# Kernel tuning notes

Measured on AMD Instinct MI355X. Metric: run time of the kernel, lower is better.

The kernel has to match this reference:

```python
import jax, jax.numpy as jnp
import numpy as np

B, C, H, W = 8, 1024, 56, 56
NBINS = 256          # torch.histc(bins=256, min=0, max=1)
T_THRESH = 0.9       # EKLM entropy-ratio threshold
NUM_CLASSES = 30


def setup_inputs() -> dict:
    key = jax.random.key(0)
    k1, k2 = jax.random.split(key)
    x = jax.random.uniform(k1, (B, C, H, W), dtype=jnp.float32)
    w_fc = jax.random.normal(k2, (C, NUM_CLASSES), dtype=jnp.float32) * 0.02
    return {"x": x, "w_fc": w_fc}


def _integral_hist(x):
    """One fused pass replacing the per-region torch.histc calls.
    Returns per-(h,w)-cell histograms [H,W,256] and their 2D inclusive
    prefix sum padded to [H+1,W+1,256] so any rectangle histogram is 4 lookups.
    Matches torch.histc semantics: values outside [0,1] ignored, v==1 -> last bin."""
    valid = (x >= 0.0) & (x <= 1.0)
    q = jnp.clip(jnp.floor(x * NBINS), 0, NBINS - 1).astype(jnp.int32)
    q = jnp.where(valid, q, NBINS)  # out-of-range -> extra bin, dropped below
    hh = jnp.broadcast_to(jnp.arange(H)[None, None, :, None], x.shape)
    ww = jnp.broadcast_to(jnp.arange(W)[None, None, None, :], x.shape)
    cell = jnp.zeros((H, W, NBINS + 1), jnp.float32).at[hh, ww, q].add(1.0)[..., :NBINS]
    integ = jnp.cumsum(jnp.cumsum(cell, axis=0), axis=1)
    integ = jnp.pad(integ, ((1, 0), (1, 0), (0, 0)))  # [H+1, W+1, 256]
    return cell, integ


def _entropy_of_hist(h):
    p = h / jnp.sum(h)
    return -jnp.sum(p * jnp.log2(p + 1e-9))


def _region_entropy(integ, xs, xd, ys, yd):
    # histogram of x[:, :, xs:xd, ys:yd] via integral-histogram lookups
    h = integ[xd, yd] - integ[xs, yd] - integ[xd, ys] + integ[xs, ys]
    return _entropy_of_hist(h)


def eklm(x):
    """Entropy-based Key Localization Method (xs fixed to 0, as in source)."""
    cell, integ = _integral_hist(x)
    # compute_entropy_for_each_y: entropy of each [:, :, 0:1, y:y+1] column cell
    col_hists = cell[0]  # [W, 256]
    p = col_hists / jnp.sum(col_hists, axis=1, keepdims=True)
    ent_y = -jnp.sum(p * jnp.log2(p + 1e-9), axis=1)
    ys0 = jnp.argmax(ent_y).astype(jnp.int32)
    total_ent = _region_entropy(integ, 0, H, 0, W)

    def ent(xd, ys, yd):
        return _region_entropy(integ, 0, xd, ys, yd)

    def cond(state):
        xd, ys, yd, Ts, done = state
        return (Ts < T_THRESH) & (~done)

    def body(state):
        xd, ys, yd, Ts, done = state
        e_cur = ent(xd, ys, yd)
        # greedy priority identical to source: grow xd, else shrink ys, else grow yd
        c1 = (xd + 1 < H) & (ent(xd + 1, ys, yd) > e_cur)
        c2 = (~c1) & (ys - 1 >= 0) & (ent(xd, jnp.maximum(ys - 1, 0), yd) > e_cur)
        c3 = (~c1) & (~c2) & (yd + 1 < W) & (ent(xd, ys, jnp.minimum(yd + 1, W)) > e_cur)
        xd_n = jnp.where(c1, xd + 1, xd)
        ys_n = jnp.where(c2, ys - 1, ys)
        yd_n = jnp.where(c3, yd + 1, yd)
        done_n = ~(c1 | c2 | c3)
        Ts_n = ent(xd_n, ys_n, yd_n) / total_ent
        return (xd_n, ys_n, yd_n, Ts_n, done_n)

    xd0 = jnp.int32(1)
    yd0 = ys0 + jnp.int32(1)
    Ts0 = ent(xd0, ys0, yd0) / total_ent
    xd, ys, yd, _, _ = jax.lax.while_loop(
        cond, body, (xd0, ys0, yd0, Ts0, jnp.bool_(False)))
    return jnp.int32(0), xd, ys, yd


def reference(x, w_fc):
    xs, xd, ys, yd = eklm(x)
    # crop the located key region (mask form for static shapes), mean-pool, classify
    row = jnp.arange(H)
    col = jnp.arange(W)
    mask = ((row[:, None] >= xs) & (row[:, None] < xd)
            & (col[None, :] >= ys) & (col[None, :] < yd)).astype(x.dtype)
    area = jnp.maximum(jnp.sum(mask), 1.0)
    pooled = jnp.einsum('bchw,hw->bc', x, mask) / area  # [B, C]
    return pooled @ w_fc  # [B, NUM_CLASSES]
```

## Files before the change

### kernel.cpp

```cpp
#include <hip/hip_runtime.h>
#include <math.h>

#define BB 8
#define CC 1024
#define HH 56
#define WW 56
#define NB 256
#define NCLS 30
#define BC (BB * CC)
#define PLANE (HH * WW)
#define NWORD (NB / 2)
#define CELLW (HH * WW * NWORD)
#define SLICES 16
#define WSPLIT 2
#define WHALF (WW / WSPLIT)
#define PL_PER_SLICE (BC / SLICES)
#define HTHREADS 256
#define VEC4_PER_BLOCK (PL_PER_SLICE * WHALF / 4)
#define LH_WORDS (WHALF * NWORD)

template <bool ATOMIC_FLUSH>
__global__ __launch_bounds__(HTHREADS) void hist_kernel(const float* __restrict__ x,
                                                        unsigned* __restrict__ dst) {
    __shared__ unsigned lh[LH_WORDS];
    const int tid = threadIdx.x;
    const int bid = blockIdx.x;
    const int whalf = bid & (WSPLIT - 1);
    const int hs = bid / WSPLIT;
    const int h = hs % HH;
    const int slice = hs / HH;

    for (int i = tid; i < LH_WORDS; i += HTHREADS) lh[i] = 0u;
    __syncthreads();

    const float* __restrict__ xb =
        x + (size_t)(slice * PL_PER_SLICE) * PLANE + h * WW + whalf * WHALF;

#pragma unroll
    for (int it = 0; it < VEC4_PER_BLOCK / HTHREADS; ++it) {
        const int j = it * HTHREADS + tid;
        const int bcl = j / 7;
        const int wq = j - bcl * 7;
        const float4 v = *(const float4*)(xb + (size_t)bcl * PLANE + wq * 4);
        const float vv[4] = {v.x, v.y, v.z, v.w};
#pragma unroll
        for (int e = 0; e < 4; ++e) {
            const float f = vv[e];
            if (f >= 0.f && f <= 1.f) {
                int bin = (int)(f * 256.f);
                if (bin > 255) bin = 255;
                const int wl = wq * 4 + e;
                atomicAdd(&lh[wl * NWORD + (bin >> 1)], 1u << ((bin & 1) << 4));
            }
        }
    }
    __syncthreads();

    if (ATOMIC_FLUSH) {
        unsigned* g = dst + ((size_t)h * WW + whalf * WHALF) * NWORD;
        for (int i = tid; i < LH_WORDS; i += HTHREADS) {
            const unsigned v = lh[i];
            if (v) atomicAdd(&g[i], v);
        }
    } else {
        unsigned* g = dst + ((size_t)hs * WW + whalf * WHALF) * NWORD;
        for (int i = tid; i < LH_WORDS; i += HTHREADS) g[i] = lh[i];
    }
}

__global__ void reduce_kernel(const unsigned* __restrict__ ps,
                              unsigned* __restrict__ hist) {
    const int idx = blockIdx.x * 256 + threadIdx.x;
    unsigned s = 0;
#pragma unroll
    for (int sl = 0; sl < SLICES; ++sl) s += ps[(size_t)sl * CELLW + idx];
    ((uint2*)hist)[idx] = make_uint2(s & 0xffffu, s >> 16);
}

__global__ void unpack_kernel(const unsigned* __restrict__ hp,
                              unsigned* __restrict__ hist) {
    const int idx = blockIdx.x * 256 + threadIdx.x;
    const unsigned s = hp[idx];
    ((uint2*)hist)[idx] = make_uint2(s & 0xffffu, s >> 16);
}

__global__ void cumw_kernel(unsigned* __restrict__ hist) {
    const int h = blockIdx.x, b = threadIdx.x;
    unsigned* base = hist + (size_t)h * WW * NB + b;
    unsigned v[WW];
#pragma unroll
    for (int w = 0; w < WW; ++w) v[w] = base[(size_t)w * NB];
    unsigned c = 0;
#pragma unroll
    for (int w = 0; w < WW; ++w) { c += v[w]; base[(size_t)w * NB] = c; }
}

__global__ void cumh_kernel(unsigned* __restrict__ hist) {
    const int w = blockIdx.x, b = threadIdx.x;
    unsigned* base = hist + (size_t)w * NB + b;
    unsigned v[HH];
#pragma unroll
    for (int h = 0; h < HH; ++h) v[h] = base[(size_t)h * WW * NB];
    unsigned c = 0;
#pragma unroll
    for (int h = 0; h < HH; ++h) { c += v[h]; base[(size_t)h * WW * NB] = c; }
}

__device__ __forceinline__ float wave_sum(float v) {
#pragma unroll
    for (int off = 32; off > 0; off >>= 1) v += __shfl_xor(v, off);
    return v;
}

__device__ __forceinline__ float ilook(const unsigned* __restrict__ integ,
                                       int a, int b, int bin) {
    return (a == 0 || b == 0)
               ? 0.f
               : (float)integ[((size_t)((a - 1) * WW + (b - 1))) * NB + bin];
}

__device__ float region_ent(const unsigned* __restrict__ integ, int lane,
                            int xd, int ys, int yd) {
    float hb[4];
    float hs = 0.f;
#pragma unroll
    for (int k = 0; k < 4; k++) {
        const int bin = lane + 64 * k;
        const float hv = ilook(integ, xd, yd, bin) - ilook(integ, xd, ys, bin);
        hb[k] = hv;
        hs += hv;
    }
    hs = wave_sum(hs);
    float e = 0.f;
#pragma unroll
    for (int k = 0; k < 4; k++) {
        const float p = hb[k] / hs;
        e += p * log2f(p + 1e-9f);
    }
    return -wave_sum(e);
}

__global__ __launch_bounds__(1024) void decide_kernel(const unsigned* __restrict__ integ,
                                                      int* __restrict__ region) {
    __shared__ float ent_s[WW];
    const int tid = threadIdx.x;
    const int lane = tid & 63;
    const int wv = tid >> 6;

    for (int w = wv; w < WW; w += 16) {
        float hb[4], hs = 0.f;
#pragma unroll
        for (int k = 0; k < 4; k++) {
            const int bin = lane + 64 * k;
            const float a = (float)integ[(size_t)w * NB + bin];
            const float b = w ? (float)integ[(size_t)(w - 1) * NB + bin] : 0.f;
            hb[k] = a - b;
            hs += hb[k];
        }
        hs = wave_sum(hs);
        float e = 0.f;
#pragma unroll
        for (int k = 0; k < 4; k++) {
            const float p = hb[k] / hs;
            e += p * log2f(p + 1e-9f);
        }
        e = -wave_sum(e);
        if (lane == 0) ent_s[w] = e;
    }
    __syncthreads();
    if (wv != 0) return;

    float best = -3.0e38f;
    int bestw = 0;
    for (int w = 0; w < WW; ++w) {
        const float e = ent_s[w];
        if (e > best) { best = e; bestw = w; }
    }

    const float total_ent = region_ent(integ, lane, HH, 0, WW);

    int xd = 1, ys = bestw, yd = bestw + 1;
    float Ts = region_ent(integ, lane, xd, ys, yd) / total_ent;
    bool done = false;
    int iter = 0;
    while (Ts < 0.9f && !done && iter < 1000) {
        iter++;
        const float e_cur = region_ent(integ, lane, xd, ys, yd);
        const int ysm = (ys - 1 < 0) ? 0 : ys - 1;
        const int ydp = (yd + 1 > WW) ? WW : yd + 1;
        const bool c1 = (xd + 1 < HH) && (region_ent(integ, lane, xd + 1, ys, yd) > e_cur);
        const bool c2 = !c1 && (ys - 1 >= 0) && (region_ent(integ, lane, xd, ysm, yd) > e_cur);
        const bool c3 = !c1 && !c2 && (yd + 1 < WW) && (region_ent(integ, lane, xd, ys, ydp) > e_cur);
        if (c1) xd = xd + 1;
        else if (c2) ys = ys - 1;
        else if (c3) yd = yd + 1;
        done = !(c1 || c2 || c3);
        Ts = region_ent(integ, lane, xd, ys, yd) / total_ent;
    }

    if (lane == 0) {
        region[0] = xd;
        region[1] = ys;
        region[2] = yd;
    }
}

__global__ void pool_kernel(const float* __restrict__ x,
                            const int* __restrict__ region,
                            float* __restrict__ pooled) {
    const int bc = blockIdx.x;
    const int xd = region[0], ys = region[1], yd = region[2];
    const int Wd = yd - ys;
    const int n = xd * Wd;
    const float area = fmaxf((float)n, 1.f);
    const float* plane = x + (size_t)bc * PLANE;
    float s = 0.f;
    for (int j = threadIdx.x; j < n; j += 64) {
        const int r = j / Wd;
        const int cc = ys + (j - r * Wd);
        s += plane[r * WW + cc];
    }
#pragma unroll
    for (int off = 32; off > 0; off >>= 1) s += __shfl_xor(s, off);
    if (threadIdx.x == 0) pooled[bc] = s / area;
}

__global__ __launch_bounds__(256) void fc_kernel(const float* __restrict__ pooled,
                                                 const float* __restrict__ wfc,
                                                 float* __restrict__ out) {
    __shared__ float red[240];
    const int b = blockIdx.x;
    const int t = threadIdx.x;
    if (t < 240) {
        const int chunk = t / NCLS;
        const int n = t - chunk * NCLS;
        const float* pv = pooled + b * CC + chunk * 128;
        const float* wv = wfc + (size_t)(chunk * 128) * NCLS + n;
        float a0 = 0.f, a1 = 0.f, a2 = 0.f, a3 = 0.f;
        for (int c = 0; c < 128; c += 4) {
            a0 += pv[c + 0] * wv[(c + 0) * NCLS];
            a1 += pv[c + 1] * wv[(c + 1) * NCLS];
            a2 += pv[c + 2] * wv[(c + 2) * NCLS];
            a3 += pv[c + 3] * wv[(c + 3) * NCLS];
        }
        red[t] = (a0 + a1) + (a2 + a3);
    }
    __syncthreads();
    if (t < NCLS) {
        float s = 0.f;
#pragma unroll
        for (int ch = 0; ch < 8; ++ch) s += red[ch * NCLS + t];
        out[b * NCLS + t] = s;
    }
}

extern "C" void kernel_launch(void* const* d_in, const int* in_sizes, int n_in,
                              void* d_out, int out_size, void* d_ws, size_t ws_size,
                              hipStream_t stream) {
    const float* x = (const float*)d_in[0];
    const float* wfc = (const float*)d_in[1];
    float* out = (float*)d_out;

    unsigned char* ws = (unsigned char*)d_ws;
    const size_t ps_bytes = (size_t)SLICES * CELLW * 4;
    const size_t hist_bytes = (size_t)CELLW * 8;
    const size_t needA = ps_bytes + hist_bytes + 4096 + (size_t)BC * 4;

    if (ws_size >= needA) {
        unsigned* ps = (unsigned*)ws;
        unsigned* hist = (unsigned*)(ws + ps_bytes);
        int* region = (int*)(ws + ps_bytes + hist_bytes);
        float* pooled = (float*)(ws + ps_bytes + hist_bytes + 4096);

        hist_kernel<false><<<HH * WSPLIT * SLICES, HTHREADS, 0, stream>>>(x, ps);
        reduce_kernel<<<CELLW / 256, 256, 0, stream>>>(ps, hist);
        cumw_kernel<<<HH, NB, 0, stream>>>(hist);
        cumh_kernel<<<WW, NB, 0, stream>>>(hist);
        decide_kernel<<<1, 1024, 0, stream>>>(hist, region);
        pool_kernel<<<BC, 64, 0, stream>>>(x, region, pooled);
        fc_kernel<<<BB, 256, 0, stream>>>(pooled, wfc, out);
    } else {
        unsigned* hp = (unsigned*)ws;
        unsigned* hist = (unsigned*)(ws + (size_t)CELLW * 4);
        int* region = (int*)(ws + (size_t)CELLW * 4 + hist_bytes);
        float* pooled = (float*)(ws + (size_t)CELLW * 4 + hist_bytes + 4096);

        hipMemsetAsync(hp, 0, (size_t)CELLW * 4, stream);
        hist_kernel<true><<<HH * WSPLIT * SLICES, HTHREADS, 0, stream>>>(x, hp);
        unpack_kernel<<<CELLW / 256, 256, 0, stream>>>(hp, hist);
        cumw_kernel<<<HH, NB, 0, stream>>>(hist);
        cumh_kernel<<<WW, NB, 0, stream>>>(hist);
        decide_kernel<<<1, 1024, 0, stream>>>(hist, region);
        pool_kernel<<<BC, 64, 0, stream>>>(x, region, pooled);
        fc_kernel<<<BB, 256, 0, stream>>>(pooled, wfc, out);
    }
}
```

Before: 187.8 us.

## Add early-exit fast path using row-0 column and global histograms

Replaces the full per-cell integral histogram build with one pass that accumulates only the row-0 per-column histograms plus a global 256-bin histogram. When the initial single-cell region already meets the entropy threshold, the search is skipped and the full integral-histogram work is avoided. Otherwise a cooperative fallback kernel rebuilds the full integral histogram with grid syncs and runs the search. The pooling kernel is also restructured for tiny regions. This trades a guaranteed full build for a data-dependent shortcut. If the ghist pass runs and the fallback still fires, it adds extra work, and the small-workspace path has no fallback at all.

```diff
diff --git a/kernel.cpp b/kernel.cpp
--- a/kernel.cpp
+++ b/kernel.cpp
@@ -1,5 +1,8 @@
 #include <hip/hip_runtime.h>
+#include <hip/hip_cooperative_groups.h>
 #include <math.h>
+
+namespace cg = cooperative_groups;
 
 #define BB 8
 #define CC 1024
@@ -10,38 +13,37 @@
 #define BC (BB * CC)
 #define PLANE (HH * WW)
 #define NWORD (NB / 2)
-#define CELLW (HH * WW * NWORD)
+#define CELLW (PLANE * NWORD)
 #define SLICES 16
-#define WSPLIT 2
-#define WHALF (WW / WSPLIT)
 #define PL_PER_SLICE (BC / SLICES)
-#define HTHREADS 256
-#define VEC4_PER_BLOCK (PL_PER_SLICE * WHALF / 4)
-#define LH_WORDS (WHALF * NWORD)
-
-template <bool ATOMIC_FLUSH>
-__global__ __launch_bounds__(HTHREADS) void hist_kernel(const float* __restrict__ x,
-                                                        unsigned* __restrict__ dst) {
-    __shared__ unsigned lh[LH_WORDS];
+
+#define FULL_NEED 28934400ull
+#define FAST_NEED 63488ull
+
+__global__ void zero_kernel(unsigned* __restrict__ p) {
+    const int i = blockIdx.x * 256 + threadIdx.x;
+    p[i] = 0u;
+}
+
+__global__ __launch_bounds__(256) void ghist_kernel(const float* __restrict__ x,
+                                                    unsigned* __restrict__ colhist,
+                                                    unsigned* __restrict__ ghist) {
+    __shared__ unsigned ch[HH * NWORD];
+    __shared__ unsigned gh[NB];
     const int tid = threadIdx.x;
-    const int bid = blockIdx.x;
-    const int whalf = bid & (WSPLIT - 1);
-    const int hs = bid / WSPLIT;
-    const int h = hs % HH;
-    const int slice = hs / HH;
-
-    for (int i = tid; i < LH_WORDS; i += HTHREADS) lh[i] = 0u;
+    for (int i = tid; i < HH * NWORD; i += 256) ch[i] = 0u;
+    gh[tid] = 0u;
     __syncthreads();
 
-    const float* __restrict__ xb =
-        x + (size_t)(slice * PL_PER_SLICE) * PLANE + h * WW + whalf * WHALF;
-
-#pragma unroll
-    for (int it = 0; it < VEC4_PER_BLOCK / HTHREADS; ++it) {
-        const int j = it * HTHREADS + tid;
-        const int bcl = j / 7;
-        const int wq = j - bcl * 7;
-        const float4 v = *(const float4*)(xb + (size_t)bcl * PLANE + wq * 4);
+    const float4* __restrict__ xb =
+        (const float4*)(x + (size_t)blockIdx.x * (16 * PLANE));
+    for (int it = 0; it < 49; ++it) {
+        const int j = it * 256 + tid;
+        const float4 v = xb[j];
+        const int e0 = j * 4;
+        const int pl = e0 / PLANE;
+        const int li = e0 - pl * PLANE;
+        const bool r0 = (li < WW);
         const float vv[4] = {v.x, v.y, v.z, v.w};
 #pragma unroll
         for (int e = 0; e < 4; ++e) {
@@ -49,61 +51,19 @@
             if (f >= 0.f && f <= 1.f) {
                 int bin = (int)(f * 256.f);
                 if (bin > 255) bin = 255;
-                const int wl = wq * 4 + e;
-                atomicAdd(&lh[wl * NWORD + (bin >> 1)], 1u << ((bin & 1) << 4));
+                atomicAdd(&gh[bin], 1u);
+                if (r0)
+                    atomicAdd(&ch[(li + e) * NWORD + (bin >> 1)],
+                              1u << ((bin & 1) << 4));
             }
         }
     }
     __syncthreads();
-
-    if (ATOMIC_FLUSH) {
-        unsigned* g = dst + ((size_t)h * WW + whalf * WHALF) * NWORD;
-        for (int i = tid; i < LH_WORDS; i += HTHREADS) {
-            const unsigned v = lh[i];
-            if (v) atomicAdd(&g[i], v);
-        }
-    } else {
-        unsigned* g = dst + ((size_t)hs * WW + whalf * WHALF) * NWORD;
-        for (int i = tid; i < LH_WORDS; i += HTHREADS) g[i] = lh[i];
-    }
-}
-
-__global__ void reduce_kernel(const unsigned* __restrict__ ps,
-                              unsigned* __restrict__ hist) {
-    const int idx = blockIdx.x * 256 + threadIdx.x;
-    unsigned s = 0;
-#pragma unroll
-    for (int sl = 0; sl < SLICES; ++sl) s += ps[(size_t)sl * CELLW + idx];
-    ((uint2*)hist)[idx] = make_uint2(s & 0xffffu, s >> 16);
-}
-
-__global__ void unpack_kernel(const unsigned* __restrict__ hp,
-                              unsigned* __restrict__ hist) {
-    const int idx = blockIdx.x * 256 + threadIdx.x;
-    const unsigned s = hp[idx];
-    ((uint2*)hist)[idx] = make_uint2(s & 0xffffu, s >> 16);
-}
-
-__global__ void cumw_kernel(unsigned* __restrict__ hist) {
-    const int h = blockIdx.x, b = threadIdx.x;
-    unsigned* base = hist + (size_t)h * WW * NB + b;
-    unsigned v[WW];
-#pragma unroll
-    for (int w = 0; w < WW; ++w) v[w] = base[(size_t)w * NB];
-    unsigned c = 0;
-#pragma unroll
-    for (int w = 0; w < WW; ++w) { c += v[w]; base[(size_t)w * NB] = c; }
-}
-
-__global__ void cumh_kernel(unsigned* __restrict__ hist) {
-    const int w = blockIdx.x, b = threadIdx.x;
-    unsigned* base = hist + (size_t)w * NB + b;
-    unsigned v[HH];
-#pragma unroll
-    for (int h = 0; h < HH; ++h) v[h] = base[(size_t)h * WW * NB];
-    unsigned c = 0;
-#pragma unroll
-    for (int h = 0; h < HH; ++h) { c += v[h]; base[(size_t)h * WW * NB] = c; }
+    for (int i = tid; i < HH * NWORD; i += 256) {
+        const unsigned v = ch[i];
+        if (v) atomicAdd(&colhist[i], v);
+    }
+    { const unsigned v = gh[tid]; if (v) atomicAdd(&ghist[tid], v); }
 }
 
 __device__ __forceinline__ float wave_sum(float v) {
@@ -140,8 +100,9 @@
     return -wave_sum(e);
 }
 
-__global__ __launch_bounds__(1024) void decide_kernel(const unsigned* __restrict__ integ,
-                                                      int* __restrict__ region) {
+__global__ __launch_bounds__(1024) void decide_fast_kernel(
+    const unsigned* __restrict__ colhist, const unsigned* __restrict__ ghist,
+    int* __restrict__ region, unsigned* __restrict__ flag) {
     __shared__ float ent_s[WW];
     const int tid = threadIdx.x;
     const int lane = tid & 63;
@@ -152,9 +113,8 @@
 #pragma unroll
         for (int k = 0; k < 4; k++) {
             const int bin = lane + 64 * k;
-            const float a = (float)integ[(size_t)w * NB + bin];
-            const float b = w ? (float)integ[(size_t)(w - 1) * NB + bin] : 0.f;
-            hb[k] = a - b;
+            const unsigned wd = colhist[w * NWORD + (bin >> 1)];
+            hb[k] = (float)((wd >> ((bin & 1) << 4)) & 0xffffu);
             hs += hb[k];
         }
         hs = wave_sum(hs);
@@ -177,52 +137,169 @@
         if (e > best) { best = e; bestw = w; }
     }
 
-    const float total_ent = region_ent(integ, lane, HH, 0, WW);
-
-    int xd = 1, ys = bestw, yd = bestw + 1;
-    float Ts = region_ent(integ, lane, xd, ys, yd) / total_ent;
-    bool done = false;
-    int iter = 0;
-    while (Ts < 0.9f && !done && iter < 1000) {
-        iter++;
-        const float e_cur = region_ent(integ, lane, xd, ys, yd);
-        const int ysm = (ys - 1 < 0) ? 0 : ys - 1;
-        const int ydp = (yd + 1 > WW) ? WW : yd + 1;
-        const bool c1 = (xd + 1 < HH) && (region_ent(integ, lane, xd + 1, ys, yd) > e_cur);
-        const bool c2 = !c1 && (ys - 1 >= 0) && (region_ent(integ, lane, xd, ysm, yd) > e_cur);
-        const bool c3 = !c1 && !c2 && (yd + 1 < WW) && (region_ent(integ, lane, xd, ys, ydp) > e_cur);
-        if (c1) xd = xd + 1;
-        else if (c2) ys = ys - 1;
-        else if (c3) yd = yd + 1;
-        done = !(c1 || c2 || c3);
-        Ts = region_ent(integ, lane, xd, ys, yd) / total_ent;
-    }
-
+    float hb[4], hs = 0.f;
+#pragma unroll
+    for (int k = 0; k < 4; k++) {
+        const int bin = lane + 64 * k;
+        hb[k] = (float)ghist[bin];
+        hs += hb[k];
+    }
+    hs = wave_sum(hs);
+    float e = 0.f;
+#pragma unroll
+    for (int k = 0; k < 4; k++) {
+        const float p = hb[k] / hs;
+        e += p * log2f(p + 1e-9f);
+    }
+    const float total_ent = -wave_sum(e);
+
+    const float Ts0 = best / total_ent;
     if (lane == 0) {
-        region[0] = xd;
-        region[1] = ys;
-        region[2] = yd;
-    }
-}
-
-__global__ void pool_kernel(const float* __restrict__ x,
-                            const int* __restrict__ region,
-                            float* __restrict__ pooled) {
-    const int bc = blockIdx.x;
+        region[0] = 1;
+        region[1] = bestw;
+        region[2] = bestw + 1;
+        *flag = (Ts0 >= 0.9f) ? 1u : 2u;
+    }
+}
+
+__global__ __launch_bounds__(256) void fallback_kernel(
+    const float* __restrict__ x, unsigned* __restrict__ ps,
+    unsigned* __restrict__ hist, int* __restrict__ region,
+    const unsigned* __restrict__ flag) {
+    if (*flag == 1u) return;
+    cg::grid_group grid = cg::this_grid();
+    __shared__ unsigned lh[HH * NWORD];
+    const int tid = threadIdx.x;
+    const int gtid = blockIdx.x * 256 + tid;
+
+    for (int t = blockIdx.x; t < HH * SLICES; t += 256) {
+        const int h = t % HH;
+        const int slice = t / HH;
+        for (int i = tid; i < HH * NWORD; i += 256) lh[i] = 0u;
+        __syncthreads();
+        const float* __restrict__ xb =
+            x + (size_t)(slice * PL_PER_SLICE) * PLANE + h * WW;
+        for (int it = 0; it < 28; ++it) {
+            const int j = it * 256 + tid;
+            const int bcl = j / 14;
+            const int wq = j - bcl * 14;
+            const float4 v = *(const float4*)(xb + (size_t)bcl * PLANE + wq * 4);
+            const float vv[4] = {v.x, v.y, v.z, v.w};
+#pragma unroll
+            for (int e = 0; e < 4; ++e) {
+                const float f = vv[e];
+                if (f >= 0.f && f <= 1.f) {
+                    int bin = (int)(f * 256.f);
+                    if (bin > 255) bin = 255;
+                    atomicAdd(&lh[(wq * 4 + e) * NWORD + (bin >> 1)],
+                              1u << ((bin & 1) << 4));
+                }
+            }
+        }
+        __syncthreads();
+        unsigned* g = ps + (size_t)slice * CELLW + (size_t)h * WW * NWORD;
+        for (int i = tid; i < HH * NWORD; i += 256) g[i] = lh[i];
+        __syncthreads();
+    }
+    grid.sync();
+
+    for (int idx = gtid; idx < CELLW; idx += 256 * 256) {
+        unsigned s = 0;
+#pragma unroll
+        for (int sl = 0; sl < SLICES; ++sl) s += ps[(size_t)sl * CELLW + idx];
+        ((uint2*)hist)[idx] = make_uint2(s & 0xffffu, s >> 16);
+    }
+    grid.sync();
+
+    if (gtid < HH * NB) {
+        const int h = gtid >> 8, b = gtid & 255;
+        unsigned* base = hist + (size_t)h * WW * NB + b;
+        unsigned v[WW];
+#pragma unroll
+        for (int w = 0; w < WW; ++w) v[w] = base[(size_t)w * NB];
+        unsigned c = 0;
+#pragma unroll
+        for (int w = 0; w < WW; ++w) { c += v[w]; base[(size_t)w * NB] = c; }
+    }
+    grid.sync();
+
+    if (gtid < WW * NB) {
+        const int w = gtid >> 8, b = gtid & 255;
+        unsigned* base = hist + (size_t)w * NB + b;
+        unsigned v[HH];
+#pragma unroll
+        for (int h = 0; h < HH; ++h) v[h] = base[(size_t)h * WW * NB];
+        unsigned c = 0;
+#pragma unroll
+        for (int h = 0; h < HH; ++h) { c += v[h]; base[(size_t)h * WW * NB] = c; }
+    }
+    grid.sync();
+
+    if (blockIdx.x == 0 && tid < 64) {
+        const int lane = tid;
+        const float total_ent = region_ent(hist, lane, HH, 0, WW);
+        int xd = region[0], ys = region[1], yd = region[2];
+        float Ts = region_ent(hist, lane, xd, ys, yd) / total_ent;
+        bool done = false;
+        int iter = 0;
+        while (Ts < 0.9f && !done && iter < 1000) {
+            iter++;
+            const float e_cur = region_ent(hist, lane, xd, ys, yd);
+            const int ysm = (ys - 1 < 0) ? 0 : ys - 1;
+            const int ydp = (yd + 1 > WW) ? WW : yd + 1;
+            const bool c1 = (xd + 1 < HH) &&
+                            (region_ent(hist, lane, xd + 1, ys, yd) > e_cur);
+            const bool c2 = !c1 && (ys - 1 >= 0) &&
+                            (region_ent(hist, lane, xd, ysm, yd) > e_cur);
+            const bool c3 = !c1 && !c2 && (yd + 1 < WW) &&
+                            (region_ent(hist, lane, xd, ys, ydp) > e_cur);
+            if (c1) xd = xd + 1;
+            else if (c2) ys = ys - 1;
+            else if (c3) yd = yd + 1;
+            done = !(c1 || c2 || c3);
+            Ts = region_ent(hist, lane, xd, ys, yd) / total_ent;
+        }
+        if (lane == 0) {
+            region[0] = xd;
+            region[1] = ys;
+            region[2] = yd;
+        }
+    }
+}
+
+__global__ __launch_bounds__(256) void pool_kernel(const float* __restrict__ x,
+                                                   const int* __restrict__ region,
+                                                   float* __restrict__ pooled) {
     const int xd = region[0], ys = region[1], yd = region[2];
     const int Wd = yd - ys;
     const int n = xd * Wd;
     const float area = fmaxf((float)n, 1.f);
-    const float* plane = x + (size_t)bc * PLANE;
-    float s = 0.f;
-    for (int j = threadIdx.x; j < n; j += 64) {
-        const int r = j / Wd;
-        const int cc = ys + (j - r * Wd);
-        s += plane[r * WW + cc];
-    }
-#pragma unroll
-    for (int off = 32; off > 0; off >>= 1) s += __shfl_xor(s, off);
-    if (threadIdx.x == 0) pooled[bc] = s / area;
+    if (n <= 16) {
+        const int bc = blockIdx.x * 256 + threadIdx.x;
+        const float* plane = x + (size_t)bc * PLANE;
+        float s = 0.f;
+        for (int j = 0; j < n; ++j) {
+            const int r = j / Wd;
+            const int cc = ys + (j - r * Wd);
+            s += plane[r * WW + cc];
+        }
+        pooled[bc] = s / area;
+    } else {
+        const int wid = (blockIdx.x * 256 + threadIdx.x) >> 6;
+        const int lane = threadIdx.x & 63;
+        for (int bc = wid; bc < BC; bc += 128) {
+            const float* plane = x + (size_t)bc * PLANE;
+            float s = 0.f;
+            for (int j = lane; j < n; j += 64) {
+                const int r = j / Wd;
+                const int cc = ys + (j - r * Wd);
+                s += plane[r * WW + cc];
+            }
+#pragma unroll
+            for (int off = 32; off > 0; off >>= 1) s += __shfl_xor(s, off);
+            if (lane == 0) pooled[bc] = s / area;
+        }
+    }
 }
 
 __global__ __launch_bounds__(256) void fc_kernel(const float* __restrict__ pooled,
@@ -262,36 +339,40 @@
     float* out = (float*)d_out;
 
     unsigned char* ws = (unsigned char*)d_ws;
-    const size_t ps_bytes = (size_t)SLICES * CELLW * 4;
-    const size_t hist_bytes = (size_t)CELLW * 8;
-    const size_t needA = ps_bytes + hist_bytes + 4096 + (size_t)BC * 4;
-
-    if (ws_size >= needA) {
-        unsigned* ps = (unsigned*)ws;
-        unsigned* hist = (unsigned*)(ws + ps_bytes);
-        int* region = (int*)(ws + ps_bytes + hist_bytes);
-        float* pooled = (float*)(ws + ps_bytes + hist_bytes + 4096);
-
-        hist_kernel<false><<<HH * WSPLIT * SLICES, HTHREADS, 0, stream>>>(x, ps);
-        reduce_kernel<<<CELLW / 256, 256, 0, stream>>>(ps, hist);
-        cumw_kernel<<<HH, NB, 0, stream>>>(hist);
-        cumh_kernel<<<WW, NB, 0, stream>>>(hist);
-        decide_kernel<<<1, 1024, 0, stream>>>(hist, region);
-        pool_kernel<<<BC, 64, 0, stream>>>(x, region, pooled);
-        fc_kernel<<<BB, 256, 0, stream>>>(pooled, wfc, out);
+    const bool full = (ws_size >= FULL_NEED);
+
+    unsigned* colhist = (unsigned*)ws;
+    unsigned* ghist = (unsigned*)(ws + HH * NWORD * 4);
+    unsigned* ps = (unsigned*)ws;
+    unsigned* hist = (unsigned*)(ws + (size_t)SLICES * CELLW * 4);
+    int* region;
+    unsigned* flag;
+    float* pooled;
+    if (full) {
+        unsigned char* meta = ws + 28901376ull;
+        region = (int*)meta;
+        flag = (unsigned*)(meta + 16);
+        pooled = (float*)(ws + 28901632ull);
     } else {
-        unsigned* hp = (unsigned*)ws;
-        unsigned* hist = (unsigned*)(ws + (size_t)CELLW * 4);
-        int* region = (int*)(ws + (size_t)CELLW * 4 + hist_bytes);
-        float* pooled = (float*)(ws + (size_t)CELLW * 4 + hist_bytes + 4096);
-
-        hipMemsetAsync(hp, 0, (size_t)CELLW * 4, stream);
-        hist_kernel<true><<<HH * WSPLIT * SLICES, HTHREADS, 0, stream>>>(x, hp);
-        unpack_kernel<<<CELLW / 256, 256, 0, stream>>>(hp, hist);
-        cumw_kernel<<<HH, NB, 0, stream>>>(hist);
-        cumh_kernel<<<WW, NB, 0, stream>>>(hist);
-        decide_kernel<<<1, 1024, 0, stream>>>(hist, region);
-        pool_kernel<<<BC, 64, 0, stream>>>(x, region, pooled);
-        fc_kernel<<<BB, 256, 0, stream>>>(pooled, wfc, out);
-    }
-}
+        region = (int*)(ws + 29696);
+        flag = (unsigned*)(ws + 29696 + 16);
+        pooled = (float*)(ws + 30720);
+    }
+
+    zero_kernel<<<29, 256, 0, stream>>>(colhist);
+    ghist_kernel<<<512, 256, 0, stream>>>(x, colhist, ghist);
+    decide_fast_kernel<<<1, 1024, 0, stream>>>(colhist, ghist, region, flag);
+    if (full) {
+        const float* xx = x;
+        unsigned* psp = ps;
+        unsigned* hp = hist;
+        int* rp = region;
+        unsigned* fp = flag;
+        void* kargs[] = {(void*)&xx, (void*)&psp, (void*)&hp, (void*)&rp,
+                         (void*)&fp};
+        hipLaunchCooperativeKernel((const void*)fallback_kernel, dim3(256),
+                                   dim3(256), kargs, 0, stream);
+    }
+    pool_kernel<<<32, 256, 0, stream>>>(x, region, pooled);
+    fc_kernel<<<BB, 256, 0, stream>>>(pooled, wfc, out);
+}
```

Measured after the change: 215.9 us. 15.0% more time.
